# Performance work log

Measured on AMD Instinct MI355X. Metric: run time of the kernel, lower is better.

Reference implementation:

```python
import jax, jax.numpy as jnp
import numpy as np

B, S, DIM = 2, 4096, 2048
H, HK, HD = 16, 8, 128          # n_heads, n_kv_heads, head_dim
M = 128                          # FAVOR random features (== head_dim)
EPS_FAVOR = 1e-6
EPS_RMS = 1e-5


def _orthogonal_random_matrix(m, d, seed=0):
    # Gaussian orthogonal random features (Performer/FAVOR+), single square block.
    rng = np.random.default_rng(seed)
    a = rng.standard_normal((d, d)).astype(np.float32)
    q, _ = np.linalg.qr(a)
    mat = q.T[:m]
    row_norms = np.linalg.norm(rng.standard_normal((m, d)).astype(np.float32), axis=1)
    return jnp.asarray(mat * row_norms[:, None], dtype=jnp.float32)


def setup_inputs() -> dict:
    key = jax.random.key(0)
    ks = jax.random.split(key, 8)
    hidden_states = jax.random.normal(ks[0], (B, S, DIM), dtype=jnp.float32)
    attention_mask = jax.random.randint(ks[1], (B, S), 0, 2).astype(jnp.int32)
    ang = jax.random.uniform(ks[2], (B, S, HD // 2), dtype=jnp.float32,
                             minval=0.0, maxval=2.0 * np.pi)
    freqs_cis = jnp.stack([jnp.cos(ang), jnp.sin(ang)], axis=-1)  # (B,S,HD/2,2)
    sc = 0.02
    wq = sc * jax.random.normal(ks[3], (H * HD, DIM), dtype=jnp.float32)
    wk = sc * jax.random.normal(ks[4], (HK * HD, DIM), dtype=jnp.float32)
    wv = sc * jax.random.normal(ks[5], (HK * HD, DIM), dtype=jnp.float32)
    wo = sc * jax.random.normal(ks[6], (DIM, H * HD), dtype=jnp.float32)
    gq = jnp.ones((HD,), dtype=jnp.float32)
    gk = jnp.ones((HD,), dtype=jnp.float32)
    proj = _orthogonal_random_matrix(M, HD, seed=0)
    return {"hidden_states": hidden_states, "attention_mask": attention_mask,
            "freqs_cis": freqs_cis, "wq": wq, "wk": wk, "wv": wv, "wo": wo,
            "gq": gq, "gk": gk, "proj": proj}


def _rmsnorm(x, w):
    return x * jax.lax.rsqrt(jnp.mean(x * x, axis=-1, keepdims=True) + EPS_RMS) * w


def _rope(x, fc):
    # x: (B,S,Hx,HD), fc: (B,S,HD/2,2) as (cos, sin); complex mult on pairs.
    xr = x.reshape(*x.shape[:-1], HD // 2, 2)
    a, b = xr[..., 0], xr[..., 1]
    c = fc[:, :, None, :, 0]
    d = fc[:, :, None, :, 1]
    out = jnp.stack([a * c - b * d, a * d + b * c], axis=-1)
    return out.reshape(x.shape)


def _favor_features(x, proj, is_query):
    # x: (B,H,S,D), proj: (M,D) -> positive random features (B,H,S,M)
    d = x.shape[-1]
    x = x * (d ** -0.25)
    xp = jnp.einsum('bhsd,md->bhsm', x, proj)
    xp = xp - 0.5 * jnp.sum(x * x, axis=-1, keepdims=True)
    if is_query:
        xp = xp - jnp.max(xp, axis=-1, keepdims=True)
    else:
        xp = xp - jnp.max(xp, axis=2, keepdims=True)
    return jnp.exp(xp) * (M ** -0.5) + EPS_FAVOR


def reference(hidden_states, attention_mask, freqs_cis, wq, wk, wv, wo, gq, gk, proj):
    x = hidden_states
    q = jnp.einsum('bsd,od->bso', x, wq).reshape(B, S, H, HD)
    k = jnp.einsum('bsd,od->bso', x, wk).reshape(B, S, HK, HD)
    v = jnp.einsum('bsd,od->bso', x, wv).reshape(B, S, HK, HD)
    q = _rmsnorm(q, gq)
    k = _rmsnorm(k, gk)
    q = _rope(q, freqs_cis)
    k = _rope(k, freqs_cis)
    # GQA: expand kv heads (repeat_interleave along head dim)
    rep = H // HK
    k = jnp.repeat(k, rep, axis=2)
    v = jnp.repeat(v, rep, axis=2)
    # (B,H,S,D)
    qh = jnp.transpose(q, (0, 2, 1, 3))
    kh = jnp.transpose(k, (0, 2, 1, 3))
    vh = jnp.transpose(v, (0, 2, 1, 3))
    valid = (attention_mask > 0).astype(jnp.float32)[:, None, :, None]  # (B,1,S,1)
    q_phi = _favor_features(qh, proj, is_query=True)   # (B,H,S,M)
    k_phi = _favor_features(kh, proj, is_query=False)  # (B,H,S,M)
    k_phi = k_phi * valid
    vh = vh * valid
    kv = jnp.einsum('bhsm,bhsd->bhmd', k_phi, vh)      # (B,H,M,D)
    k_sum = jnp.sum(k_phi, axis=2)                     # (B,H,M)
    out = jnp.einsum('bhsm,bhmd->bhsd', q_phi, kv)
    denom = jnp.einsum('bhsm,bhm->bhs', q_phi, k_sum)[..., None]
    out = out / (denom + EPS_FAVOR)
    out = out * valid
    out = jnp.transpose(out, (0, 2, 1, 3)).reshape(B, S, H * HD)
    return jnp.einsum('bso,do->bsd', out, wo)


if __name__ == '__main__':
    o = reference(**setup_inputs())
    print(o.shape, o.dtype)
```

## Files before the change

kernel.cpp:

```cpp
#include <hip/hip_runtime.h>

#define B_ 2
#define S_ 4096
#define DIM_ 2048
#define H_ 16
#define HK_ 8
#define HD_ 128
#define M_ 128

typedef unsigned short u16;
typedef __bf16 bf16x8 __attribute__((ext_vector_type(8)));
typedef float f32x4 __attribute__((ext_vector_type(4)));

__device__ __forceinline__ u16 f2b(float f) {
  unsigned u = __float_as_uint(f);
  u = u + 0x7fffu + ((u >> 16) & 1u);
  return (u16)(u >> 16);
}
__device__ __forceinline__ float b2f(u16 h) {
  return __uint_as_float(((unsigned)h) << 16);
}
__device__ __forceinline__ unsigned fenc(float f) {
  unsigned u = __float_as_uint(f);
  return (u & 0x80000000u) ? ~u : (u | 0x80000000u);
}
__device__ __forceinline__ float fdec(unsigned e) {
  unsigned u = (e & 0x80000000u) ? (e & 0x7fffffffu) : ~e;
  return __uint_as_float(u);
}

__global__ void f2b_kernel(const float* __restrict__ in, u16* __restrict__ out, int n4) {
  int i = blockIdx.x * blockDim.x + threadIdx.x;
  if (i < n4) {
    float4 v = ((const float4*)in)[i];
    ushort4 o;
    o.x = f2b(v.x); o.y = f2b(v.y); o.z = f2b(v.z); o.w = f2b(v.w);
    ((ushort4*)out)[i] = o;
  }
}

__global__ void tproj_kernel(const float* __restrict__ p, float* __restrict__ pT) {
  int i = blockIdx.x * 256 + threadIdx.x;
  int d = i >> 7, m = i & 127;
  pT[i] = p[m * 128 + d];
}

__global__ void init_kernel(float* __restrict__ kvf, unsigned* __restrict__ kmaxu,
                            float* __restrict__ ksum) {
  int i = blockIdx.x * 256 + threadIdx.x;
  if (i < B_ * HK_ * M_ * HD_) kvf[i] = 0.f;
  if (i < B_ * HK_ * M_) { kmaxu[i] = 0u; ksum[i] = 0.f; }
}

__global__ __launch_bounds__(256) void gemm_bt(
    const u16* __restrict__ A, const u16* __restrict__ Bm, float* __restrict__ C,
    int M, int N, int K,
    unsigned long long sAb, unsigned long long sBb, unsigned long long sCb,
    int bshiftB, int ldc, int ksplit)
{
  __shared__ __align__(16) u16 sA[128 * 32];
  __shared__ __align__(16) u16 sB[128 * 32];
  const int t = threadIdx.x;
  const int wave = t >> 6, lane = t & 63;
  const int z = blockIdx.z;
  const int batch = z / ksplit;
  const int ks = z - batch * ksplit;
  const int kLen = K / ksplit, kBeg = ks * kLen;

  const u16* Ab = A + (size_t)batch * sAb + (size_t)blockIdx.x * 128 * (size_t)K;
  const u16* Bb = Bm + (size_t)(batch >> bshiftB) * sBb + (size_t)blockIdx.y * 128 * (size_t)K;
  float* Cb = C + (size_t)batch * sCb + (size_t)blockIdx.x * 128 * (size_t)ldc
                + (size_t)blockIdx.y * 128;

  const int r0 = wave * 16 + (lane >> 2);
  const int e0 = (lane & 3) * 8;
  const int wr = wave >> 1, wc = wave & 1;

  f32x4 acc[4][4] = {};

  for (int k0 = kBeg; k0 < kBeg + kLen; k0 += 32) {
#pragma unroll
    for (int i = 0; i < 2; i++) {
      __builtin_amdgcn_global_load_lds(
          (const __attribute__((address_space(1))) void*)(Ab + (size_t)(r0 + i * 64) * K + k0 + e0),
          (__attribute__((address_space(3))) void*)(&sA[(i * 4 + wave) * 512]), 16, 0, 0);
      __builtin_amdgcn_global_load_lds(
          (const __attribute__((address_space(1))) void*)(Bb + (size_t)(r0 + i * 64) * K + k0 + e0),
          (__attribute__((address_space(3))) void*)(&sB[(i * 4 + wave) * 512]), 16, 0, 0);
    }
    __syncthreads();
    bf16x8 av[4], bv[4];
#pragma unroll
    for (int m = 0; m < 4; m++)
      av[m] = *(const bf16x8*)&sA[(wr * 64 + m * 16 + (lane & 15)) * 32 + (lane >> 4) * 8];
#pragma unroll
    for (int n = 0; n < 4; n++)
      bv[n] = *(const bf16x8*)&sB[(wc * 64 + n * 16 + (lane & 15)) * 32 + (lane >> 4) * 8];
#pragma unroll
    for (int m = 0; m < 4; m++)
#pragma unroll
      for (int n = 0; n < 4; n++)
        acc[m][n] = __builtin_amdgcn_mfma_f32_16x16x32_bf16(av[m], bv[n], acc[m][n], 0, 0, 0);
    __syncthreads();
  }

  const int crow0 = wr * 64 + (lane >> 4) * 4;
  const int ccol = wc * 64 + (lane & 15);
  if (ksplit == 1) {
#pragma unroll
    for (int m = 0; m < 4; m++)
#pragma unroll
      for (int n = 0; n < 4; n++)
#pragma unroll
        for (int r = 0; r < 4; r++)
          Cb[(size_t)(crow0 + m * 16 + r) * ldc + ccol + n * 16] = acc[m][n][r];
  } else {
#pragma unroll
    for (int m = 0; m < 4; m++)
#pragma unroll
      for (int n = 0; n < 4; n++)
#pragma unroll
        for (int r = 0; r < 4; r++)
          atomicAdd(&Cb[(size_t)(crow0 + m * 16 + r) * ldc + ccol + n * 16], acc[m][n][r]);
  }
}

template <int IS_Q>
__global__ __launch_bounds__(256) void favor_kernel(
    const float* __restrict__ qkv, const float* __restrict__ fc,
    const float* __restrict__ g, const float* __restrict__ pT,
    float* __restrict__ kpre, unsigned* __restrict__ kmaxu,
    u16* __restrict__ qphib, const float* __restrict__ ksum, float* __restrict__ denom,
    int colbase)
{
  const int b = blockIdx.z, h = blockIdx.y;
  const int wave = threadIdx.x >> 6, lane = threadIdx.x & 63;
  const int s0 = blockIdx.x * 16 + wave * 4;
  __shared__ float xs[4][4][128];
  float halfss[4];
  const int col = colbase + h * HD_;

#pragma unroll
  for (int tt = 0; tt < 4; tt++) {
    const int s = s0 + tt;
    const size_t row = (size_t)b * S_ + s;
    const float* xr = qkv + row * 4096 + col;
    float a = xr[2 * lane], bb = xr[2 * lane + 1];
    float ss = a * a + bb * bb;
#pragma unroll
    for (int o = 1; o < 64; o <<= 1) ss += __shfl_xor(ss, o);
    const float sc = rsqrtf(ss * (1.f / HD_) + 1e-5f);
    a *= sc * g[2 * lane];
    bb *= sc * g[2 * lane + 1];
    const float2 cs = *(const float2*)&fc[(row * 64 + lane) * 2];
    float na = a * cs.x - bb * cs.y;
    float nb = a * cs.y + bb * cs.x;
    na *= 0.29730177875068026f;
    nb *= 0.29730177875068026f;
    xs[wave][tt][2 * lane] = na;
    xs[wave][tt][2 * lane + 1] = nb;
    float s2 = na * na + nb * nb;
#pragma unroll
    for (int o = 1; o < 64; o <<= 1) s2 += __shfl_xor(s2, o);
    halfss[tt] = 0.5f * s2;
  }

  float acc[4][2] = {};
  for (int d = 0; d < 128; d++) {
    const float2 p = *(const float2*)&pT[d * 128 + 2 * lane];
#pragma unroll
    for (int tt = 0; tt < 4; tt++) {
      const float xv = xs[wave][tt][d];
      acc[tt][0] = fmaf(p.x, xv, acc[tt][0]);
      acc[tt][1] = fmaf(p.y, xv, acc[tt][1]);
    }
  }

  if (IS_Q) {
#pragma unroll
    for (int tt = 0; tt < 4; tt++) {
      const int s = s0 + tt;
      const float p0 = acc[tt][0] - halfss[tt], p1 = acc[tt][1] - halfss[tt];
      float mx = fmaxf(p0, p1);
#pragma unroll
      for (int o = 1; o < 64; o <<= 1) mx = fmaxf(mx, __shfl_xor(mx, o));
      const float f0 = expf(p0 - mx) * 0.08838834764831845f + 1e-6f;
      const float f1 = expf(p1 - mx) * 0.08838834764831845f + 1e-6f;
      const u16 u0 = f2b(f0), u1 = f2b(f1);
      const size_t base = (((size_t)(b * H_ + h)) * S_ + s) * M_;
      ushort2 st2; st2.x = u0; st2.y = u1;
      *(ushort2*)&qphib[base + 2 * lane] = st2;
      const float* ksb = ksum + ((b * HK_) + (h >> 1)) * M_;
      float dsum = b2f(u0) * ksb[2 * lane] + b2f(u1) * ksb[2 * lane + 1];
#pragma unroll
      for (int o = 1; o < 64; o <<= 1) dsum += __shfl_xor(dsum, o);
      if (lane == 0) denom[((size_t)(b * H_ + h)) * S_ + s] = dsum;
    }
  } else {
    float mx0 = -1e30f, mx1 = -1e30f;
#pragma unroll
    for (int tt = 0; tt < 4; tt++) {
      const int s = s0 + tt;
      const float p0 = acc[tt][0] - halfss[tt], p1 = acc[tt][1] - halfss[tt];
      const size_t base = (((size_t)(b * HK_ + h)) * S_ + s) * M_;
      float2 w2; w2.x = p0; w2.y = p1;
      *(float2*)&kpre[base + 2 * lane] = w2;
      mx0 = fmaxf(mx0, p0);
      mx1 = fmaxf(mx1, p1);
    }
    unsigned* km = kmaxu + (b * HK_ + h) * M_;
    atomicMax(&km[2 * lane], fenc(mx0));
    atomicMax(&km[2 * lane + 1], fenc(mx1));
  }
}

__global__ __launch_bounds__(256) void kexp_kernel(
    const float* __restrict__ kpre, const unsigned* __restrict__ kmaxu,
    const int* __restrict__ amask, u16* __restrict__ kphiT, float* __restrict__ ksum)
{
  const int b = blockIdx.z, hk = blockIdx.y;
  const int c0 = blockIdx.x * 64;
  const int t = threadIdx.x;
  const int m = t & 127, half = t >> 7;
  __shared__ __align__(16) u16 st[128][64];
  __shared__ float red[256];
  const int bhk = b * HK_ + hk;
  const float kmax = fdec(kmaxu[bhk * M_ + m]);
  float sum = 0.f;
  for (int i = 0; i < 32; i++) {
    const int sl = half * 32 + i;
    const int s = c0 + sl;
    const float pre = kpre[(((size_t)bhk) * S_ + s) * M_ + m];
    const int va = amask[b * S_ + s] > 0;
    const float phi = va ? (expf(pre - kmax) * 0.08838834764831845f + 1e-6f) : 0.f;
    sum += phi;
    st[m][sl] = f2b(phi);
  }
  red[t] = sum;
  __syncthreads();
  if (t < 128) atomicAdd(&ksum[bhk * M_ + t], red[t] + red[t + 128]);
  const int mr = t >> 1, part = t & 1;
  const size_t base = ((size_t)(bhk * M_ + mr)) * S_ + c0 + part * 32;
#pragma unroll
  for (int k = 0; k < 4; k++)
    *(uint4*)&kphiT[base + k * 8] = *(const uint4*)&st[mr][part * 32 + k * 8];
}

__global__ __launch_bounds__(256) void vT_kernel(
    const float* __restrict__ qkv, const int* __restrict__ amask, u16* __restrict__ vT)
{
  const int b = blockIdx.z, hk = blockIdx.y;
  const int c0 = blockIdx.x * 64;
  const int t = threadIdx.x;
  const int d = t & 127, half = t >> 7;
  __shared__ __align__(16) u16 st[128][64];
  const int bhk = b * HK_ + hk;
  for (int i = 0; i < 32; i++) {
    const int sl = half * 32 + i;
    const int s = c0 + sl;
    const float v = qkv[((size_t)(b * S_ + s)) * 4096 + 3072 + hk * 128 + d];
    const int va = amask[b * S_ + s] > 0;
    st[d][sl] = f2b(va ? v : 0.f);
  }
  __syncthreads();
  const int dr = t >> 1, part = t & 1;
  const size_t base = ((size_t)(bhk * 128 + dr)) * S_ + c0 + part * 32;
#pragma unroll
  for (int k = 0; k < 4; k++)
    *(uint4*)&vT[base + k * 8] = *(const uint4*)&st[dr][part * 32 + k * 8];
}

__global__ void kvb_kernel(const float* __restrict__ kvf, u16* __restrict__ kvb) {
  const int i = blockIdx.x * 256 + threadIdx.x;
  const int bhk = i >> 14;
  const int rem = i & 16383;
  const int d = rem >> 7, m = rem & 127;
  kvb[i] = f2b(kvf[(bhk << 14) + m * 128 + d]);
}

__global__ __launch_bounds__(256) void epi_kernel(
    const float* __restrict__ oraw, const float* __restrict__ denom,
    const int* __restrict__ amask, u16* __restrict__ attnb)
{
  const int tid = blockIdx.x * 256 + threadIdx.x;
  const int d4 = tid & 31;
  const int s = (tid >> 5) & (S_ - 1);
  const int h = (tid >> 17) & (H_ - 1);
  const int b = tid >> 21;
  const float den = denom[((size_t)(b * H_ + h)) * S_ + s] + 1e-6f;
  const float vm = (amask[b * S_ + s] > 0) ? 1.f : 0.f;
  const float4 v = *(const float4*)&oraw[(((size_t)(b * H_ + h)) * S_ + s) * HD_ + d4 * 4];
  const float inv = vm / den;
  ushort4 o;
  o.x = f2b(v.x * inv); o.y = f2b(v.y * inv); o.z = f2b(v.z * inv); o.w = f2b(v.w * inv);
  *(ushort4*)&attnb[((size_t)(b * S_ + s)) * 2048 + h * 128 + d4 * 4] = o;
}

extern "C" void kernel_launch(void* const* d_in, const int* in_sizes, int n_in,
                              void* d_out, int out_size, void* d_ws, size_t ws_size,
                              hipStream_t stream)
{
  const float* x  = (const float*)d_in[0];
  const int*   am = (const int*)d_in[1];
  const float* fc = (const float*)d_in[2];
  const float* wq = (const float*)d_in[3];
  const float* wk = (const float*)d_in[4];
  const float* wv = (const float*)d_in[5];
  const float* wo = (const float*)d_in[6];
  const float* gq = (const float*)d_in[7];
  const float* gk = (const float*)d_in[8];
  const float* pj = (const float*)d_in[9];
  float* out = (float*)d_out;

  char* w = (char*)d_ws;
  size_t off = 0;
  u16*   xb    = (u16*)(w + off);  off += (size_t)B_ * S_ * DIM_ * 2;
  u16*   wqkvb = (u16*)(w + off);  off += 4096ull * 2048 * 2;
  u16*   wob   = (u16*)(w + off);  off += 2048ull * 2048 * 2;
  float* qkv   = (float*)(w + off); off += (size_t)B_ * S_ * 4096 * 4;
  float* kpre  = (float*)(w + off); off += (size_t)B_ * HK_ * S_ * M_ * 4;
  u16*   kphiT = (u16*)(w + off);  off += (size_t)B_ * HK_ * S_ * M_ * 2;
  u16*   vT    = (u16*)(w + off);  off += (size_t)B_ * HK_ * S_ * HD_ * 2;
  float* kvf   = (float*)(w + off); off += (size_t)B_ * HK_ * M_ * HD_ * 4;
  u16*   kvb   = (u16*)(w + off);  off += (size_t)B_ * HK_ * M_ * HD_ * 2;
  float* pT    = (float*)(w + off); off += 128ull * 128 * 4;
  unsigned* kmaxu = (unsigned*)(w + off); off += (size_t)B_ * HK_ * M_ * 4;
  float* ksum  = (float*)(w + off); off += (size_t)B_ * HK_ * M_ * 4;
  float* denom = (float*)(w + off); off += (size_t)B_ * H_ * S_ * 4;
  u16*   attnb = xb;
  u16*   qphib = (u16*)kpre;
  if (ws_size < off) return;

  f2b_kernel<<<16384, 256, 0, stream>>>(x, xb, 4194304);
  f2b_kernel<<<4096, 256, 0, stream>>>(wq, wqkvb, 1048576);
  f2b_kernel<<<2048, 256, 0, stream>>>(wk, wqkvb + 4194304, 524288);
  f2b_kernel<<<2048, 256, 0, stream>>>(wv, wqkvb + 6291456, 524288);
  f2b_kernel<<<4096, 256, 0, stream>>>(wo, wob, 1048576);
  tproj_kernel<<<64, 256, 0, stream>>>(pj, pT);
  init_kernel<<<1024, 256, 0, stream>>>(kvf, kmaxu, ksum);

  gemm_bt<<<dim3(64, 32, 1), 256, 0, stream>>>(xb, wqkvb, qkv,
      8192, 4096, 2048, 0ull, 0ull, 0ull, 0, 4096, 1);

  favor_kernel<0><<<dim3(S_ / 16, HK_, B_), 256, 0, stream>>>(
      qkv, fc, gk, pT, kpre, kmaxu, nullptr, nullptr, nullptr, 2048);
  kexp_kernel<<<dim3(S_ / 64, HK_, B_), 256, 0, stream>>>(kpre, kmaxu, am, kphiT, ksum);
  vT_kernel<<<dim3(S_ / 64, HK_, B_), 256, 0, stream>>>(qkv, am, vT);
  favor_kernel<1><<<dim3(S_ / 16, H_, B_), 256, 0, stream>>>(
      qkv, fc, gq, pT, nullptr, nullptr, qphib, ksum, denom, 0);

  gemm_bt<<<dim3(1, 1, 256), 256, 0, stream>>>(kphiT, vT, kvf,
      128, 128, 4096, 524288ull, 524288ull, 16384ull, 0, 128, 16);
  kvb_kernel<<<1024, 256, 0, stream>>>(kvf, kvb);

  gemm_bt<<<dim3(32, 1, 32), 256, 0, stream>>>(qphib, kvb, qkv ,
      4096, 128, 128, 524288ull, 16384ull, 524288ull, 1, 128, 1);

  epi_kernel<<<16384, 256, 0, stream>>>(qkv, denom, am, attnb);

  gemm_bt<<<dim3(64, 16, 1), 256, 0, stream>>>(attnb, wob, out,
      8192, 2048, 2048, 0ull, 0ull, 0ull, 0, 2048, 1);
}
```

Measured before the change: 835.5 us.

## Add 256x256 pipelined GEMM, fuse attention epilogue, swizzle transpose LDS

Replaces the QKV and output projection GEMMs with a new 256x256-tile, 512-thread kernel. It double-buffers LDS through direct global-to-LDS loads with XOR swizzling, remaps workgroups across groups of eight, and raises wave priority around the MFMAs. The q_phi·kv GEMM is fused with the denominator/mask epilogue so the fp32 intermediate round-trip and a separate kernel launch go away. The kmax atomics in favor_kernel are pre-reduced across waves in LDS, and the transpose kernels get XOR-swizzled LDS to avoid bank conflicts. The larger tiles use 128 KB of LDS per block, which limits occupancy and gives fewer blocks for the output GEMM.

```diff
diff --git a/kernel.cpp b/kernel.cpp
--- a/kernel.cpp
+++ b/kernel.cpp
@@ -50,6 +50,113 @@
   int i = blockIdx.x * 256 + threadIdx.x;
   if (i < B_ * HK_ * M_ * HD_) kvf[i] = 0.f;
   if (i < B_ * HK_ * M_) { kmaxu[i] = 0u; ksum[i] = 0.f; }
+}
+
+__global__ __launch_bounds__(512, 2) void gemm256(
+    const u16* __restrict__ A, const u16* __restrict__ Bm, float* __restrict__ C,
+    int K, int ldc, int nbx)
+{
+  __shared__ __align__(16) u16 lds[65536];
+  const int t = threadIdx.x;
+  const int wave = t >> 6, lane = t & 63;
+  const int nwg = gridDim.x;
+  const int q8 = nwg >> 3;
+  const int id = blockIdx.x;
+  const int sid = (id & 7) * q8 + (id >> 3);
+  const int nby = nwg / nbx;
+  const int by = sid % nby;
+  const int bx = sid / nby;
+  const int wave_m = wave >> 2;
+  const int wave_n = wave & 3;
+  const int lr = lane & 15, lg = lane >> 4;
+
+  const int srow = lane >> 3;
+  const int scolE = (((lane & 7) ^ srow) << 3);
+
+  const int NT = K >> 6;
+  f32x4 acc[8][4] = {};
+
+  const u16* Abase = A + (size_t)bx * 256 * (size_t)K;
+  const u16* Bbase = Bm + (size_t)by * 256 * (size_t)K;
+
+#define STAGE256(buf, k0)                                                            \
+  {                                                                                  \
+    _Pragma("unroll")                                                                \
+    for (int sub = 0; sub < 2; sub++) {                                              \
+      const int rowH = (wave * 2 + sub) * 8 + srow;                                  \
+      const int chunk = (wave * 2 + sub) * 512;                                      \
+      _Pragma("unroll")                                                              \
+      for (int hh = 0; hh < 2; hh++) {                                               \
+        __builtin_amdgcn_global_load_lds(                                            \
+            (const __attribute__((address_space(1))) void*)(Abase + (size_t)(hh * 128 + rowH) * K + (k0) + scolE), \
+            (__attribute__((address_space(3))) void*)&lds[(buf) * 16384 + hh * 8192 + chunk], 16, 0, 0); \
+        __builtin_amdgcn_global_load_lds(                                            \
+            (const __attribute__((address_space(1))) void*)(Bbase + (size_t)(hh * 128 + rowH) * K + (k0) + scolE), \
+            (__attribute__((address_space(3))) void*)&lds[32768 + (buf) * 16384 + hh * 8192 + chunk], 16, 0, 0); \
+      }                                                                              \
+    }                                                                                \
+  }
+
+  STAGE256(0, 0);
+  __syncthreads();
+
+  for (int tt = 0; tt < NT; tt++) {
+    const int cur = tt & 1;
+    const int AbaseH = cur * 16384 + wave_m * 8192;
+    const int BbaseH = 32768 + cur * 16384 + (wave_n >> 1) * 8192;
+#pragma unroll
+    for (int q = 0; q < 4; q++) {
+      if (q == 0 && tt + 1 < NT) { STAGE256(cur ^ 1, (tt + 1) * 64) }
+      const int mh = q >> 1, nh = q & 1;
+      bf16x8 af[4][2], bfr[2][2];
+#pragma unroll
+      for (int m = 0; m < 4; m++) {
+        const int r = mh * 64 + m * 16 + lr;
+#pragma unroll
+        for (int kk = 0; kk < 2; kk++) {
+          const int cb = ((kk << 6) | (lg << 4)) ^ ((lr & 7) << 4);
+          af[m][kk] = *(const bf16x8*)&lds[AbaseH + r * 64 + (cb >> 1)];
+        }
+      }
+#pragma unroll
+      for (int n = 0; n < 2; n++) {
+        const int r = (wave_n & 1) * 64 + nh * 32 + n * 16 + lr;
+#pragma unroll
+        for (int kk = 0; kk < 2; kk++) {
+          const int cb = ((kk << 6) | (lg << 4)) ^ ((lr & 7) << 4);
+          bfr[n][kk] = *(const bf16x8*)&lds[BbaseH + r * 64 + (cb >> 1)];
+        }
+      }
+      asm volatile("" ::: "memory");
+      __builtin_amdgcn_s_barrier();
+      asm volatile("" ::: "memory");
+      __builtin_amdgcn_s_setprio(1);
+#pragma unroll
+      for (int kk = 0; kk < 2; kk++)
+#pragma unroll
+        for (int m = 0; m < 4; m++)
+#pragma unroll
+          for (int n = 0; n < 2; n++)
+            acc[mh * 4 + m][nh * 2 + n] =
+                __builtin_amdgcn_mfma_f32_16x16x32_bf16(af[m][kk], bfr[n][kk],
+                                                        acc[mh * 4 + m][nh * 2 + n], 0, 0, 0);
+      __builtin_amdgcn_s_setprio(0);
+      asm volatile("" ::: "memory");
+      if (q == 3) asm volatile("s_waitcnt vmcnt(0)" ::: "memory");
+      __builtin_amdgcn_s_barrier();
+      asm volatile("" ::: "memory");
+    }
+  }
+
+  float* Cb = C + (size_t)(bx * 256 + wave_m * 128 + lg * 4) * ldc + by * 256 + wave_n * 64 + lr;
+#pragma unroll
+  for (int i = 0; i < 8; i++)
+#pragma unroll
+    for (int j = 0; j < 4; j++)
+#pragma unroll
+      for (int r = 0; r < 4; r++)
+        Cb[(size_t)(i * 16 + r) * ldc + j * 16] = acc[i][j][r];
+#undef STAGE256
 }
 
 __global__ __launch_bounds__(256) void gemm_bt(
@@ -125,6 +232,69 @@
   }
 }
 
+__global__ __launch_bounds__(256) void gemm_out_epi(
+    const u16* __restrict__ qphib, const u16* __restrict__ kvb,
+    const float* __restrict__ denom, const int* __restrict__ amask,
+    u16* __restrict__ attnb)
+{
+  __shared__ __align__(16) u16 sA[128 * 32];
+  __shared__ __align__(16) u16 sB[128 * 32];
+  const int t = threadIdx.x;
+  const int wave = t >> 6, lane = t & 63;
+  const int batch = blockIdx.z;
+  const int b = batch >> 4, h = batch & 15;
+
+  const u16* Ab = qphib + (size_t)batch * 524288 + (size_t)blockIdx.x * 128 * 128;
+  const u16* Bb = kvb + (size_t)(batch >> 1) * 16384;
+
+  const int r0 = wave * 16 + (lane >> 2);
+  const int e0 = (lane & 3) * 8;
+  const int wr = wave >> 1, wc = wave & 1;
+
+  f32x4 acc[4][4] = {};
+
+  for (int k0 = 0; k0 < 128; k0 += 32) {
+#pragma unroll
+    for (int i = 0; i < 2; i++) {
+      __builtin_amdgcn_global_load_lds(
+          (const __attribute__((address_space(1))) void*)(Ab + (size_t)(r0 + i * 64) * 128 + k0 + e0),
+          (__attribute__((address_space(3))) void*)(&sA[(i * 4 + wave) * 512]), 16, 0, 0);
+      __builtin_amdgcn_global_load_lds(
+          (const __attribute__((address_space(1))) void*)(Bb + (size_t)(r0 + i * 64) * 128 + k0 + e0),
+          (__attribute__((address_space(3))) void*)(&sB[(i * 4 + wave) * 512]), 16, 0, 0);
+    }
+    __syncthreads();
+    bf16x8 av[4], bv[4];
+#pragma unroll
+    for (int m = 0; m < 4; m++)
+      av[m] = *(const bf16x8*)&sA[(wr * 64 + m * 16 + (lane & 15)) * 32 + (lane >> 4) * 8];
+#pragma unroll
+    for (int n = 0; n < 4; n++)
+      bv[n] = *(const bf16x8*)&sB[(wc * 64 + n * 16 + (lane & 15)) * 32 + (lane >> 4) * 8];
+#pragma unroll
+    for (int m = 0; m < 4; m++)
+#pragma unroll
+      for (int n = 0; n < 4; n++)
+        acc[m][n] = __builtin_amdgcn_mfma_f32_16x16x32_bf16(av[m], bv[n], acc[m][n], 0, 0, 0);
+    __syncthreads();
+  }
+
+  const int crow0 = wr * 64 + (lane >> 4) * 4;
+  const int ccol = wc * 64 + (lane & 15);
+#pragma unroll
+  for (int m = 0; m < 4; m++)
+#pragma unroll
+    for (int r = 0; r < 4; r++) {
+      const int s = blockIdx.x * 128 + crow0 + m * 16 + r;
+      const float inv = (amask[b * S_ + s] > 0)
+                          ? 1.f / (denom[(size_t)batch * S_ + s] + 1e-6f) : 0.f;
+      u16* orow = attnb + ((size_t)(b * S_ + s)) * 2048 + h * 128 + ccol;
+#pragma unroll
+      for (int n = 0; n < 4; n++)
+        orow[n * 16] = f2b(acc[m][n][r] * inv);
+    }
+}
+
 template <int IS_Q>
 __global__ __launch_bounds__(256) void favor_kernel(
     const float* __restrict__ qkv, const float* __restrict__ fc,
@@ -137,6 +307,7 @@
   const int wave = threadIdx.x >> 6, lane = threadIdx.x & 63;
   const int s0 = blockIdx.x * 16 + wave * 4;
   __shared__ float xs[4][4][128];
+  __shared__ float sm[4][128];
   float halfss[4];
   const int col = colbase + h * HD_;
 
@@ -208,9 +379,14 @@
       mx0 = fmaxf(mx0, p0);
       mx1 = fmaxf(mx1, p1);
     }
-    unsigned* km = kmaxu + (b * HK_ + h) * M_;
-    atomicMax(&km[2 * lane], fenc(mx0));
-    atomicMax(&km[2 * lane + 1], fenc(mx1));
+    sm[wave][2 * lane] = mx0;
+    sm[wave][2 * lane + 1] = mx1;
+    __syncthreads();
+    if (threadIdx.x < 128) {
+      const float v = fmaxf(fmaxf(sm[0][threadIdx.x], sm[1][threadIdx.x]),
+                            fmaxf(sm[2][threadIdx.x], sm[3][threadIdx.x]));
+      atomicMax(&kmaxu[(b * HK_ + h) * M_ + threadIdx.x], fenc(v));
+    }
   }
 }
 
@@ -227,6 +403,7 @@
   const int bhk = b * HK_ + hk;
   const float kmax = fdec(kmaxu[bhk * M_ + m]);
   float sum = 0.f;
+  const int msw = (m & 7) << 3;
   for (int i = 0; i < 32; i++) {
     const int sl = half * 32 + i;
     const int s = c0 + sl;
@@ -234,16 +411,17 @@
     const int va = amask[b * S_ + s] > 0;
     const float phi = va ? (expf(pre - kmax) * 0.08838834764831845f + 1e-6f) : 0.f;
     sum += phi;
-    st[m][sl] = f2b(phi);
+    st[m][sl ^ msw] = f2b(phi);
   }
   red[t] = sum;
   __syncthreads();
   if (t < 128) atomicAdd(&ksum[bhk * M_ + t], red[t] + red[t + 128]);
   const int mr = t >> 1, part = t & 1;
+  const int rsw = (mr & 7) << 3;
   const size_t base = ((size_t)(bhk * M_ + mr)) * S_ + c0 + part * 32;
 #pragma unroll
   for (int k = 0; k < 4; k++)
-    *(uint4*)&kphiT[base + k * 8] = *(const uint4*)&st[mr][part * 32 + k * 8];
+    *(uint4*)&kphiT[base + k * 8] = *(const uint4*)&st[mr][(part * 32 + k * 8) ^ rsw];
 }
 
 __global__ __launch_bounds__(256) void vT_kernel(
@@ -255,19 +433,21 @@
   const int d = t & 127, half = t >> 7;
   __shared__ __align__(16) u16 st[128][64];
   const int bhk = b * HK_ + hk;
+  const int dsw = (d & 7) << 3;
   for (int i = 0; i < 32; i++) {
     const int sl = half * 32 + i;
     const int s = c0 + sl;
     const float v = qkv[((size_t)(b * S_ + s)) * 4096 + 3072 + hk * 128 + d];
     const int va = amask[b * S_ + s] > 0;
-    st[d][sl] = f2b(va ? v : 0.f);
+    st[d][sl ^ dsw] = f2b(va ? v : 0.f);
   }
   __syncthreads();
   const int dr = t >> 1, part = t & 1;
+  const int rsw = (dr & 7) << 3;
   const size_t base = ((size_t)(bhk * 128 + dr)) * S_ + c0 + part * 32;
 #pragma unroll
   for (int k = 0; k < 4; k++)
-    *(uint4*)&vT[base + k * 8] = *(const uint4*)&st[dr][part * 32 + k * 8];
+    *(uint4*)&vT[base + k * 8] = *(const uint4*)&st[dr][(part * 32 + k * 8) ^ rsw];
 }
 
 __global__ void kvb_kernel(const float* __restrict__ kvf, u16* __restrict__ kvb) {
@@ -276,24 +456,6 @@
   const int rem = i & 16383;
   const int d = rem >> 7, m = rem & 127;
   kvb[i] = f2b(kvf[(bhk << 14) + m * 128 + d]);
-}
-
-__global__ __launch_bounds__(256) void epi_kernel(
-    const float* __restrict__ oraw, const float* __restrict__ denom,
-    const int* __restrict__ amask, u16* __restrict__ attnb)
-{
-  const int tid = blockIdx.x * 256 + threadIdx.x;
-  const int d4 = tid & 31;
-  const int s = (tid >> 5) & (S_ - 1);
-  const int h = (tid >> 17) & (H_ - 1);
-  const int b = tid >> 21;
-  const float den = denom[((size_t)(b * H_ + h)) * S_ + s] + 1e-6f;
-  const float vm = (amask[b * S_ + s] > 0) ? 1.f : 0.f;
-  const float4 v = *(const float4*)&oraw[(((size_t)(b * H_ + h)) * S_ + s) * HD_ + d4 * 4];
-  const float inv = vm / den;
-  ushort4 o;
-  o.x = f2b(v.x * inv); o.y = f2b(v.y * inv); o.z = f2b(v.z * inv); o.w = f2b(v.w * inv);
-  *(ushort4*)&attnb[((size_t)(b * S_ + s)) * 2048 + h * 128 + d4 * 4] = o;
 }
 
 extern "C" void kernel_launch(void* const* d_in, const int* in_sizes, int n_in,
@@ -339,8 +501,7 @@
   tproj_kernel<<<64, 256, 0, stream>>>(pj, pT);
   init_kernel<<<1024, 256, 0, stream>>>(kvf, kmaxu, ksum);
 
-  gemm_bt<<<dim3(64, 32, 1), 256, 0, stream>>>(xb, wqkvb, qkv,
-      8192, 4096, 2048, 0ull, 0ull, 0ull, 0, 4096, 1);
+  gemm256<<<512, 512, 0, stream>>>(xb, wqkvb, qkv, 2048, 4096, 32);
 
   favor_kernel<0><<<dim3(S_ / 16, HK_, B_), 256, 0, stream>>>(
       qkv, fc, gk, pT, kpre, kmaxu, nullptr, nullptr, nullptr, 2048);
@@ -353,11 +514,7 @@
       128, 128, 4096, 524288ull, 524288ull, 16384ull, 0, 128, 16);
   kvb_kernel<<<1024, 256, 0, stream>>>(kvf, kvb);
 
-  gemm_bt<<<dim3(32, 1, 32), 256, 0, stream>>>(qphib, kvb, qkv ,
-      4096, 128, 128, 524288ull, 16384ull, 524288ull, 1, 128, 1);
-
-  epi_kernel<<<16384, 256, 0, stream>>>(qkv, denom, am, attnb);
-
-  gemm_bt<<<dim3(64, 16, 1), 256, 0, stream>>>(attnb, wob, out,
-      8192, 2048, 2048, 0ull, 0ull, 0ull, 0, 2048, 1);
-}
+  gemm_out_epi<<<dim3(32, 1, 32), 256, 0, stream>>>(qphib, kvb, denom, am, attnb);
+
+  gemm256<<<256, 512, 0, stream>>>(attnb, wob, out, 2048, 2048, 32);
+}
```

Result: faster. 694.4 us (-16.9%).
